# Kernel tuning notes

Hardware: AMD Instinct MI355X
Metric: run time of the kernel (lower is better)

Reference implementation:

```python
import jax, jax.numpy as jnp
import numpy as np

C_DIM = 512
N_TOKEN = 256
N_HEADS = 8
TOKEN_DIM = C_DIM // N_HEADS  # 64


def setup_inputs() -> dict:
    key = jax.random.key(0)
    ks = jax.random.split(key, 8)
    s = 1.0 / np.sqrt(C_DIM)
    W0 = jax.random.normal(ks[0], (4, 8192, C_DIM), dtype=jnp.float32)
    # learnable query tokens (xavier-uniform-ish)
    lim = np.sqrt(6.0 / (N_TOKEN + TOKEN_DIM))
    Q = jax.random.uniform(ks[1], (N_HEADS, N_TOKEN, TOKEN_DIM), minval=-lim, maxval=lim, dtype=jnp.float32)
    kv1_w = jax.random.normal(ks[2], (C_DIM, C_DIM), dtype=jnp.float32) * s
    kv1_b = jnp.zeros((C_DIM,), dtype=jnp.float32)
    qkv2_w = jax.random.normal(ks[3], (TOKEN_DIM, 2 * TOKEN_DIM), dtype=jnp.float32) * (1.0 / np.sqrt(TOKEN_DIM))
    q3_w = jax.random.normal(ks[4], (C_DIM, C_DIM), dtype=jnp.float32) * s
    q3_b = jnp.zeros((C_DIM,), dtype=jnp.float32)
    proj_w = jax.random.normal(ks[5], (C_DIM, C_DIM), dtype=jnp.float32) * s
    proj_b = jnp.zeros((C_DIM,), dtype=jnp.float32)
    return {"W0": W0, "Q": Q, "kv1_w": kv1_w, "kv1_b": kv1_b, "qkv2_w": qkv2_w,
            "q3_w": q3_w, "q3_b": q3_b, "proj_w": proj_w, "proj_b": proj_b}


def reference(W0, Q, kv1_w, kv1_b, qkv2_w, q3_w, q3_b, proj_w, proj_b):
    b, n, c = W0.shape
    h, td = N_HEADS, TOKEN_DIM
    scale = 1.0 / np.sqrt(td)
    # stage 1: compress n nodes into n_token tokens per head
    kv1 = (W0 @ kv1_w + kv1_b).reshape(b, n, h, td).transpose(0, 2, 1, 3)  # b h n c
    pw = jnp.einsum('hmc,bhnc->bhmn', Q, kv1) * scale
    pw = jax.nn.softmax(pw, axis=-1)
    proj_token = jnp.einsum('bhmn,bhnc->bhmc', pw, kv1)  # b h m c
    # stage 2: re-project tokens back to nodes
    kv2 = proj_token @ qkv2_w  # b h m 2c
    k, v = kv2[..., :td], kv2[..., td:]
    q3 = (W0 @ q3_w + q3_b).reshape(b, n, h, td).transpose(0, 2, 1, 3)  # b h n c
    rw = jax.nn.softmax(jnp.einsum('bhnc,bhmc->bhnm', q3, k) * scale, axis=-1)
    W = jnp.einsum('bhnm,bhmc->bhnc', rw, v)
    W = W.transpose(0, 2, 1, 3).reshape(b, n, c)  # b n (h c)
    return W @ proj_w + proj_b
```

## Files before the change

### kernel.cpp

```cpp
#include <hip/hip_runtime.h>
#include <hip/hip_bf16.h>


#define NB 4
#define NSEQ 8192
#define CD 512
#define NH 8
#define TD 64
#define NTOK 256
#define NSPLIT 16
#define NKEYS (NSEQ / NSPLIT)

typedef unsigned short u16;
typedef unsigned int u32;
typedef __bf16 bf16x8 __attribute__((ext_vector_type(8)));
typedef float f32x4 __attribute__((ext_vector_type(4)));
typedef float f32x16 __attribute__((ext_vector_type(16)));

__device__ __forceinline__ u16 f2bf(float f){
  __hip_bfloat16 h = __float2bfloat16(f);
  u16 u; __builtin_memcpy(&u, &h, 2); return u;
}
__device__ __forceinline__ bf16x8 ld8(const u16* p){
  bf16x8 r; __builtin_memcpy(&r, p, 16); return r;
}
__device__ __forceinline__ f32x4 mfma16(bf16x8 a, bf16x8 b, f32x4 c){
  return __builtin_amdgcn_mfma_f32_16x16x32_bf16(a, b, c, 0, 0, 0);
}
__device__ __forceinline__ f32x16 mfma32(bf16x8 a, bf16x8 b, f32x16 c){
  return __builtin_amdgcn_mfma_f32_32x32x16_bf16(a, b, c, 0, 0, 0);
}

__global__ void k_cvt(const float* __restrict__ W0, u16* __restrict__ W0b){
  size_t i = (size_t)blockIdx.x * 256 + threadIdx.x;
  float4 v = ((const float4*)W0)[i];
  u16 w[4] = { f2bf(v.x), f2bf(v.y), f2bf(v.z), f2bf(v.w) };
  __builtin_memcpy(W0b + i*4, w, 8);
}

__global__ void k_prep(const float* __restrict__ kv1_w, const float* __restrict__ q3_w,
                       const float* __restrict__ proj_w, const float* __restrict__ Q,
                       u16* __restrict__ kv1_wt, u16* __restrict__ q3_wt,
                       u16* __restrict__ proj_wt, u16* __restrict__ Qb){
  int i = blockIdx.x * 256 + threadIdx.x;
  int k = i >> 9, n = i & 511;
  kv1_wt [n*CD + k] = f2bf(kv1_w[i]);
  q3_wt  [n*CD + k] = f2bf(q3_w[i] * 0.125f);
  proj_wt[n*CD + k] = f2bf(proj_w[i]);
  if (i < NH*NTOK*TD) Qb[i] = f2bf(Q[i] * 0.125f);
}

__global__ __launch_bounds__(256, 2)
void k_gemm_dual(const u16* __restrict__ A, const u16* __restrict__ B1t,
                 const u16* __restrict__ B2t, const float* __restrict__ bias1,
                 const float* __restrict__ bias2, float bscale2,
                 u16* __restrict__ out1, u16* __restrict__ out2){
  __shared__ __attribute__((aligned(16))) u16 As[128][72];
  __shared__ __attribute__((aligned(16))) u16 B1s[128][72];
  __shared__ __attribute__((aligned(16))) u16 B2s[128][72];
  const int tid = threadIdx.x;
  const int lane = tid & 63, wave = tid >> 6;
  const int l15 = lane & 15, lg = lane >> 4;
  const int wm = (wave >> 1) * 64, wn = (wave & 1) * 64;
  const int bm = blockIdx.x, bn = blockIdx.y;
  f32x4 acc1[4][4] = {}, acc2[4][4] = {};

#pragma unroll 1
  for (int k0 = 0; k0 < CD; k0 += 64){
    __syncthreads();
    {
      int r0 = tid >> 3, c8 = (tid & 7) << 3;
#pragma unroll
      for (int rr = 0; rr < 128; rr += 32){
        const u16* srcA = A   + (size_t)(bm*128 + r0 + rr) * CD + k0 + c8;
        int4 va = *(const int4*)srcA;
        __builtin_memcpy(&As[r0 + rr][c8], &va, 16);
        const u16* s1 = B1t + (size_t)(bn*128 + r0 + rr) * CD + k0 + c8;
        int4 v1 = *(const int4*)s1;
        __builtin_memcpy(&B1s[r0 + rr][c8], &v1, 16);
        const u16* s2 = B2t + (size_t)(bn*128 + r0 + rr) * CD + k0 + c8;
        int4 v2 = *(const int4*)s2;
        __builtin_memcpy(&B2s[r0 + rr][c8], &v2, 16);
      }
    }
    __syncthreads();
#pragma unroll
    for (int ks = 0; ks < 2; ks++){
      bf16x8 af[4], b1f[4], b2f[4];
#pragma unroll
      for (int mf = 0; mf < 4; mf++) af[mf]  = ld8(&As[wm + mf*16 + l15][ks*32 + lg*8]);
#pragma unroll
      for (int nf = 0; nf < 4; nf++){
        b1f[nf] = ld8(&B1s[wn + nf*16 + l15][ks*32 + lg*8]);
        b2f[nf] = ld8(&B2s[wn + nf*16 + l15][ks*32 + lg*8]);
      }
#pragma unroll
      for (int mf = 0; mf < 4; mf++)
#pragma unroll
        for (int nf = 0; nf < 4; nf++){
          acc1[mf][nf] = mfma16(af[mf], b1f[nf], acc1[mf][nf]);
          acc2[mf][nf] = mfma16(af[mf], b2f[nf], acc2[mf][nf]);
        }
    }
  }
#pragma unroll
  for (int nf = 0; nf < 4; nf++){
    int col = bn*128 + wn + nf*16 + l15;
    float bv1 = bias1[col];
    float bv2 = bias2[col] * bscale2;
#pragma unroll
    for (int mf = 0; mf < 4; mf++){
      int row = bm*128 + wm + mf*16 + lg*4;
#pragma unroll
      for (int q = 0; q < 4; q++){
        out1[(size_t)(row + q)*CD + col] = f2bf(acc1[mf][nf][q] + bv1);
        out2[(size_t)(row + q)*CD + col] = f2bf(acc2[mf][nf][q] + bv2);
      }
    }
  }
}

template<int OUT_F32>
__global__ __launch_bounds__(256, 2)
void k_gemm512(const u16* __restrict__ A, const u16* __restrict__ Bt,
               const float* __restrict__ bias, float bscale, void* __restrict__ outp){
  __shared__ __attribute__((aligned(16))) u16 As[128][72];
  __shared__ __attribute__((aligned(16))) u16 Bs[128][72];
  const int tid = threadIdx.x;
  const int lane = tid & 63, wave = tid >> 6;
  const int l15 = lane & 15, lg = lane >> 4;
  const int wm = (wave >> 1) * 64, wn = (wave & 1) * 64;
  const int bm = blockIdx.x, bn = blockIdx.y;
  f32x4 acc[4][4] = {};

#pragma unroll 1
  for (int k0 = 0; k0 < CD; k0 += 64){
    __syncthreads();
    {
      int r0 = tid >> 3, c8 = (tid & 7) << 3;
#pragma unroll
      for (int rr = 0; rr < 128; rr += 32){
        const u16* srcA = A  + (size_t)(bm*128 + r0 + rr) * CD + k0 + c8;
        int4 va = *(const int4*)srcA;
        __builtin_memcpy(&As[r0 + rr][c8], &va, 16);
        const u16* srcB = Bt + (size_t)(bn*128 + r0 + rr) * CD + k0 + c8;
        int4 vb = *(const int4*)srcB;
        __builtin_memcpy(&Bs[r0 + rr][c8], &vb, 16);
      }
    }
    __syncthreads();
#pragma unroll
    for (int ks = 0; ks < 2; ks++){
      bf16x8 af[4], bfr[4];
#pragma unroll
      for (int mf = 0; mf < 4; mf++) af[mf]  = ld8(&As[wm + mf*16 + l15][ks*32 + lg*8]);
#pragma unroll
      for (int nf = 0; nf < 4; nf++) bfr[nf] = ld8(&Bs[wn + nf*16 + l15][ks*32 + lg*8]);
#pragma unroll
      for (int mf = 0; mf < 4; mf++)
#pragma unroll
        for (int nf = 0; nf < 4; nf++)
          acc[mf][nf] = mfma16(af[mf], bfr[nf], acc[mf][nf]);
    }
  }
#pragma unroll
  for (int nf = 0; nf < 4; nf++){
    int col = bn*128 + wn + nf*16 + l15;
    float bv = bias[col] * bscale;
#pragma unroll
    for (int mf = 0; mf < 4; mf++){
      int row = bm*128 + wm + mf*16 + lg*4;
#pragma unroll
      for (int q = 0; q < 4; q++){
        float v = acc[mf][nf][q] + bv;
        if constexpr (OUT_F32) ((float*)outp)[(size_t)(row + q)*CD + col] = v;
        else                   ((u16*)outp)[(size_t)(row + q)*CD + col] = f2bf(v);
      }
    }
  }
}

__global__ __launch_bounds__(256, 4)
void k_attn1(const u16* __restrict__ kv1, const u16* __restrict__ Qb,
             float* __restrict__ o_part, float* __restrict__ ml_part){
  __shared__ __attribute__((aligned(16))) u16 kvs[64][72];
  __shared__ __attribute__((aligned(16))) u16 kvts[64][72];
  __shared__ __attribute__((aligned(16))) u16 pws[4][32][72];
  const int tid = threadIdx.x, lane = tid & 63, wave = tid >> 6;
  const int bh = blockIdx.x, mt = blockIdx.y, s = blockIdx.z;
  const int b = bh >> 3, h = bh & 7;
  const int l15 = lane & 15, lg = lane >> 4;
  const int m0 = mt*128 + wave*32;

  bf16x8 qf[2][2];
#pragma unroll
  for (int mf = 0; mf < 2; mf++)
#pragma unroll
    for (int ks = 0; ks < 2; ks++)
      qf[mf][ks] = ld8(Qb + (size_t)(h*NTOK + m0 + mf*16 + l15)*TD + ks*32 + lg*8);

  float mst[2][4], lst[2][4];
  f32x4 oac[2][4] = {};
#pragma unroll
  for (int mf = 0; mf < 2; mf++)
#pragma unroll
    for (int q = 0; q < 4; q++){ mst[mf][q] = -1e30f; lst[mf][q] = 0.f; }

#pragma unroll 1
  for (int c = 0; c < NKEYS/64; c++){
    const int nc = s*NKEYS + c*64;
    __syncthreads();
    {
      int r = tid >> 2, seg = (tid & 3) * 16;
      const u16* src = kv1 + (size_t)(b*NSEQ + nc + r)*CD + h*TD + seg;
      int4 v0 = *(const int4*)src;
      int4 v1 = *(const int4*)(src + 8);
      __builtin_memcpy(&kvs[r][seg],     &v0, 16);
      __builtin_memcpy(&kvs[r][seg + 8], &v1, 16);
      u16 tmp[16];
      __builtin_memcpy(tmp,     &v0, 16);
      __builtin_memcpy(tmp + 8, &v1, 16);
#pragma unroll
      for (int j = 0; j < 16; j++) kvts[seg + j][r] = tmp[j];
    }
    __syncthreads();
    f32x4 d[2][4] = {};
#pragma unroll
    for (int nf = 0; nf < 4; nf++)
#pragma unroll
      for (int ks = 0; ks < 2; ks++){
        bf16x8 kf = ld8(&kvs[nf*16 + l15][ks*32 + lg*8]);
#pragma unroll
        for (int mf = 0; mf < 2; mf++) d[mf][nf] = mfma16(qf[mf][ks], kf, d[mf][nf]);
      }
#pragma unroll
    for (int mf = 0; mf < 2; mf++)
#pragma unroll
      for (int q = 0; q < 4; q++){
        float cm = fmaxf(fmaxf(d[mf][0][q], d[mf][1][q]), fmaxf(d[mf][2][q], d[mf][3][q]));
#pragma unroll
        for (int off = 1; off < 16; off <<= 1) cm = fmaxf(cm, __shfl_xor(cm, off, 64));
        float mnew = fmaxf(mst[mf][q], cm);
        float corr = __expf(mst[mf][q] - mnew);
        float rs = 0.f;
#pragma unroll
        for (int nf = 0; nf < 4; nf++){
          float e = __expf(d[mf][nf][q] - mnew);
          d[mf][nf][q] = e; rs += e;
        }
#pragma unroll
        for (int off = 1; off < 16; off <<= 1) rs += __shfl_xor(rs, off, 64);
        lst[mf][q] = lst[mf][q]*corr + rs;
        mst[mf][q] = mnew;
#pragma unroll
        for (int tf = 0; tf < 4; tf++) oac[mf][tf][q] *= corr;
        int ml = mf*16 + lg*4 + q;
#pragma unroll
        for (int nf = 0; nf < 4; nf++) pws[wave][ml][nf*16 + l15] = f2bf(d[mf][nf][q]);
      }
#pragma unroll
    for (int ks = 0; ks < 2; ks++){
      bf16x8 a[2];
#pragma unroll
      for (int mf = 0; mf < 2; mf++) a[mf] = ld8(&pws[wave][mf*16 + l15][ks*32 + lg*8]);
#pragma unroll
      for (int tf = 0; tf < 4; tf++){
        bf16x8 vf = ld8(&kvts[tf*16 + l15][ks*32 + lg*8]);
#pragma unroll
        for (int mf = 0; mf < 2; mf++) oac[mf][tf] = mfma16(a[mf], vf, oac[mf][tf]);
      }
    }
  }
  const size_t pbase = (size_t)(bh*NSPLIT + s);
#pragma unroll
  for (int mf = 0; mf < 2; mf++)
#pragma unroll
    for (int q = 0; q < 4; q++){
      int m = m0 + mf*16 + lg*4 + q;
#pragma unroll
      for (int tf = 0; tf < 4; tf++)
        o_part[(pbase*NTOK + m)*TD + tf*16 + l15] = oac[mf][tf][q];
      if (l15 == 0){
        ml_part[(pbase*2)*NTOK + m]     = mst[mf][q];
        ml_part[(pbase*2 + 1)*NTOK + m] = lst[mf][q];
      }
    }
}

__global__ __launch_bounds__(256, 2)
void k_comb(const float* __restrict__ o_part, const float* __restrict__ ml_part,
            const float* __restrict__ qkv2_w, u16* __restrict__ kb, u16* __restrict__ vtb){
  __shared__ float w2[TD*2*TD];
  __shared__ float osh[16][68];
  const int tid = threadIdx.x;
  const int bh = blockIdx.x >> 4, mtile = blockIdx.x & 15;
  const int m0 = mtile * 16;
  for (int i = tid; i < TD*2*TD/4; i += 256) ((float4*)w2)[i] = ((const float4*)qkv2_w)[i];

  const int mi = tid >> 4, tj = tid & 15;
  const int m = m0 + mi;
  float M = -1e30f;
#pragma unroll
  for (int s = 0; s < NSPLIT; s++)
    M = fmaxf(M, ml_part[(size_t)((bh*NSPLIT + s)*2)*NTOK + m]);
  float4 acc = make_float4(0.f,0.f,0.f,0.f);
  float denom = 0.f;
#pragma unroll 1
  for (int s = 0; s < NSPLIT; s++){
    size_t base = (size_t)(bh*NSPLIT + s);
    float w = __expf(ml_part[(base*2)*NTOK + m] - M);
    denom += ml_part[(base*2 + 1)*NTOK + m] * w;
    float4 v = ((const float4*)(o_part + (base*NTOK + m)*TD))[tj];
    acc.x += w*v.x; acc.y += w*v.y; acc.z += w*v.z; acc.w += w*v.w;
  }
  float inv = 1.f / denom;
  osh[mi][tj*4+0] = acc.x*inv; osh[mi][tj*4+1] = acc.y*inv;
  osh[mi][tj*4+2] = acc.z*inv; osh[mi][tj*4+3] = acc.w*inv;
  __syncthreads();
  const int j0 = tj * 8;
  float o8[8] = {};
#pragma unroll
  for (int t = 0; t < TD; t++){
    float ov = osh[mi][t];
#pragma unroll
    for (int jj = 0; jj < 8; jj++) o8[jj] += ov * w2[t*2*TD + j0 + jj];
  }
  if (j0 < TD){
#pragma unroll
    for (int jj = 0; jj < 8; jj++)
      kb[(size_t)(bh*NTOK + m)*TD + j0 + jj] = f2bf(o8[jj]);
  } else {
#pragma unroll
    for (int jj = 0; jj < 8; jj++)
      vtb[(size_t)(bh*TD + (j0 - TD + jj))*NTOK + m] = f2bf(o8[jj]);
  }
}

__global__ __launch_bounds__(256, 2)
void k_attn2(const u16* __restrict__ q3, const u16* __restrict__ kb,
             const u16* __restrict__ vtb, u16* __restrict__ Wout){
  __shared__ __attribute__((aligned(16))) u16 buf[32768];
  u16* kbs = buf;
  u16* vts = buf + 16384;
  const int tid = threadIdx.x, lane = tid & 63, wave = tid >> 6;
  const int bh = blockIdx.x >> 6, nt = blockIdx.x & 63;
  const int b = bh >> 3, h = bh & 7;
  const int l31 = lane & 31, hi = lane >> 5;
  const int n0 = nt * 128 + wave * 32;

  bf16x8 bq[4];
#pragma unroll
  for (int ks = 0; ks < 4; ks++)
    bq[ks] = ld8(q3 + (size_t)(b*NSEQ + n0 + l31)*CD + h*TD + ks*16 + hi*8);

  {
    const u16* ksrc = kb + (size_t)bh*NTOK*TD;
#pragma unroll
    for (int it = 0; it < 8; it++){
      int idx = it*256 + tid;
      int r = idx >> 3, g = idx & 7;
      int4 v; __builtin_memcpy(&v, ksrc + r*64 + g*8, 16);
      __builtin_memcpy(kbs + r*64 + ((g ^ (r & 7)) << 3), &v, 16);
    }
    const u16* vsrc = vtb + (size_t)bh*TD*NTOK;
#pragma unroll
    for (int it = 0; it < 8; it++){
      int idx = it*256 + tid;
      int t = idx >> 5, g = idx & 31;
      int4 v; __builtin_memcpy(&v, vsrc + t*256 + g*8, 16);
      __builtin_memcpy(vts + t*256 + ((g ^ (t & 31)) << 3), &v, 16);
    }
  }
  __syncthreads();

  f32x16 p[8] = {};
  __builtin_amdgcn_s_setprio(1);
#pragma unroll
  for (int kt = 0; kt < 8; kt++){
#pragma unroll
    for (int ks = 0; ks < 4; ks++){
      int r = kt*32 + l31, g = ks*2 + hi;
      bf16x8 ak = ld8(kbs + r*64 + ((g ^ (r & 7)) << 3));
      p[kt] = mfma32(ak, bq[ks], p[kt]);
    }
  }
  __builtin_amdgcn_s_setprio(0);

  float mx0 = -1e30f, mx1 = -1e30f, mx2 = -1e30f, mx3 = -1e30f;
#pragma unroll
  for (int kt = 0; kt < 8; kt++){
#pragma unroll
    for (int r = 0; r < 16; r += 4){
      mx0 = fmaxf(mx0, p[kt][r+0]); mx1 = fmaxf(mx1, p[kt][r+1]);
      mx2 = fmaxf(mx2, p[kt][r+2]); mx3 = fmaxf(mx3, p[kt][r+3]);
    }
  }
  float m = fmaxf(fmaxf(mx0, mx1), fmaxf(mx2, mx3));
  m = fmaxf(m, __shfl_xor(m, 32, 64));
  float s0 = 0.f, s1 = 0.f, s2 = 0.f, s3 = 0.f;
#pragma unroll
  for (int kt = 0; kt < 8; kt++){
#pragma unroll
    for (int r = 0; r < 16; r += 4){
      float e0 = __expf(p[kt][r+0] - m); p[kt][r+0] = e0; s0 += e0;
      float e1 = __expf(p[kt][r+1] - m); p[kt][r+1] = e1; s1 += e1;
      float e2 = __expf(p[kt][r+2] - m); p[kt][r+2] = e2; s2 += e2;
      float e3 = __expf(p[kt][r+3] - m); p[kt][r+3] = e3; s3 += e3;
    }
  }
  float rs = (s0 + s1) + (s2 + s3);
  rs += __shfl_xor(rs, 32, 64);
  const float inv = 1.f / rs;

  f32x16 o0 = {}, o1 = {};
#pragma unroll
  for (int kt = 0; kt < 8; kt++){
    u32 w[8], x[8];
#pragma unroll
    for (int j = 0; j < 8; j++){
      u32 lo = f2bf(p[kt][2*j]);
      u32 hh = f2bf(p[kt][2*j + 1]);
      w[j] = lo | (hh << 16);
    }
#pragma unroll
    for (int j = 0; j < 8; j++) x[j] = __shfl_xor(w[j], 32, 64);
    __builtin_amdgcn_s_setprio(1);
#pragma unroll
    for (int c = 0; c < 2; c++){
      u32 arr[4];
      arr[0] = hi ? x[4*c + 2] : w[4*c + 0];
      arr[1] = hi ? x[4*c + 3] : w[4*c + 1];
      arr[2] = hi ? w[4*c + 2] : x[4*c + 0];
      arr[3] = hi ? w[4*c + 3] : x[4*c + 1];
      bf16x8 pb; __builtin_memcpy(&pb, arr, 16);
      int g = kt*4 + c*2 + hi;
      bf16x8 av0 = ld8(vts + l31*256        + ((g ^ l31) << 3));
      bf16x8 av1 = ld8(vts + (l31+32)*256   + ((g ^ l31) << 3));
      o0 = mfma32(av0, pb, o0);
      o1 = mfma32(av1, pb, o1);
    }
    __builtin_amdgcn_s_setprio(0);
  }

  __syncthreads();
  u16 (*osh)[32][68] = (u16 (*)[32][68])buf;
#pragma unroll
  for (int r = 0; r < 16; r++){
    int row = (r & 3) + 8*(r >> 2) + 4*hi;
    osh[wave][l31][row]      = f2bf(o0[r] * inv);
    osh[wave][l31][32 + row] = f2bf(o1[r] * inv);
  }
  const u16* src = &osh[wave][l31][hi*32];
  int4 v0, v1, v2, v3;
  __builtin_memcpy(&v0, src,      16);
  __builtin_memcpy(&v1, src + 8,  16);
  __builtin_memcpy(&v2, src + 16, 16);
  __builtin_memcpy(&v3, src + 24, 16);
  u16* dst = Wout + (size_t)(b*NSEQ + n0 + l31)*CD + h*TD + hi*32;
  __builtin_memcpy(dst,      &v0, 16);
  __builtin_memcpy(dst + 8,  &v1, 16);
  __builtin_memcpy(dst + 16, &v2, 16);
  __builtin_memcpy(dst + 24, &v3, 16);
}

extern "C" void kernel_launch(void* const* d_in, const int* in_sizes, int n_in,
                              void* d_out, int out_size, void* d_ws, size_t ws_size,
                              hipStream_t stream){
  const float* W0     = (const float*)d_in[0];
  const float* Q      = (const float*)d_in[1];
  const float* kv1_w  = (const float*)d_in[2];
  const float* kv1_b  = (const float*)d_in[3];
  const float* qkv2_w = (const float*)d_in[4];
  const float* q3_w   = (const float*)d_in[5];
  const float* q3_b   = (const float*)d_in[6];
  const float* proj_w = (const float*)d_in[7];
  const float* proj_b = (const float*)d_in[8];
  (void)in_sizes; (void)n_in; (void)out_size; (void)ws_size;

  char* ws = (char*)d_ws;
  u16*   W0b     = (u16*)  (ws);
  u16*   kv1_ws  = (u16*)  (ws + ((size_t)32<<20));
  float* o_part  = (float*)(ws + ((size_t)64<<20));
  float* ml_part = (float*)(ws + ((size_t)96<<20));
  u16*   kv1_wt  = (u16*)  (ws + ((size_t)97<<20));
  u16*   q3_wt   = (u16*)  (ws + ((size_t)97<<20) + (1<<19));
  u16*   proj_wt = (u16*)  (ws + ((size_t)98<<20));
  u16*   Qb      = (u16*)  (ws + ((size_t)98<<20) + (1<<19));
  u16*   kb      = (u16*)  (ws + ((size_t)99<<20));
  u16*   vtb     = (u16*)  (ws + ((size_t)100<<20));
  u16*   W_ws    = (u16*)  (ws + ((size_t)32<<20));
  u16*   q3s     = (u16*)  d_out;

  k_cvt<<<16384, 256, 0, stream>>>(W0, W0b);
  k_prep<<<1024, 256, 0, stream>>>(kv1_w, q3_w, proj_w, Q, kv1_wt, q3_wt, proj_wt, Qb);
  k_gemm_dual<<<dim3(256,4), 256, 0, stream>>>(W0b, kv1_wt, q3_wt, kv1_b, q3_b, 0.125f,
                                               kv1_ws, q3s);
  k_attn1<<<dim3(NB*NH, 2, NSPLIT), 256, 0, stream>>>(kv1_ws, Qb, o_part, ml_part);
  k_comb<<<NB*NH*16, 256, 0, stream>>>(o_part, ml_part, qkv2_w, kb, vtb);
  k_attn2<<<NB*NH*64, 256, 0, stream>>>(q3s, kb, vtb, W_ws);
  k_gemm512<1><<<dim3(256,4), 256, 0, stream>>>(W_ws, proj_wt, proj_b, 1.0f, (void*)d_out);
}
```

Before: 217.1 us.

## Rewrite stage-1 attention with 32x32 MFMA and register-resident softmax probabilities

Restructures the k_attn1 flash-attention loop to use 32x32x16 MFMAs with S transposed (keys as rows), so each lane holds the scores for one query column. Softmax probabilities are converted to bf16 and exchanged between half-waves with a single shuffle, which removes the per-wave LDS staging buffer and the 16-lane shuffle reductions. It also adds a lazy rescale that only updates the running max when it grows by more than 8, and staggers the transposed LDS writes to reduce bank conflicts. Occupancy launch bounds drop from 4 to 3 blocks per CU to allow more registers. The lazy rescale relies on fp32 headroom for exponentials up to e^8.

```diff
diff --git a/kernel.cpp b/kernel.cpp
--- a/kernel.cpp
+++ b/kernel.cpp
@@ -180,38 +180,31 @@
   }
 }
 
-__global__ __launch_bounds__(256, 4)
+__global__ __launch_bounds__(256, 3)
 void k_attn1(const u16* __restrict__ kv1, const u16* __restrict__ Qb,
              float* __restrict__ o_part, float* __restrict__ ml_part){
   __shared__ __attribute__((aligned(16))) u16 kvs[64][72];
   __shared__ __attribute__((aligned(16))) u16 kvts[64][72];
-  __shared__ __attribute__((aligned(16))) u16 pws[4][32][72];
   const int tid = threadIdx.x, lane = tid & 63, wave = tid >> 6;
   const int bh = blockIdx.x, mt = blockIdx.y, s = blockIdx.z;
   const int b = bh >> 3, h = bh & 7;
-  const int l15 = lane & 15, lg = lane >> 4;
+  const int l31 = lane & 31, hi = lane >> 5;
   const int m0 = mt*128 + wave*32;
 
-  bf16x8 qf[2][2];
-#pragma unroll
-  for (int mf = 0; mf < 2; mf++)
-#pragma unroll
-    for (int ks = 0; ks < 2; ks++)
-      qf[mf][ks] = ld8(Qb + (size_t)(h*NTOK + m0 + mf*16 + l15)*TD + ks*32 + lg*8);
-
-  float mst[2][4], lst[2][4];
-  f32x4 oac[2][4] = {};
-#pragma unroll
-  for (int mf = 0; mf < 2; mf++)
-#pragma unroll
-    for (int q = 0; q < 4; q++){ mst[mf][q] = -1e30f; lst[mf][q] = 0.f; }
+  bf16x8 bq[4];
+#pragma unroll
+  for (int ks = 0; ks < 4; ks++)
+    bq[ks] = ld8(Qb + (size_t)(h*NTOK + m0 + l31)*TD + ks*16 + hi*8);
+
+  float mrun = -1e30f, srun = 0.f;
+  f32x16 o0 = {}, o1 = {};
 
 #pragma unroll 1
   for (int c = 0; c < NKEYS/64; c++){
     const int nc = s*NKEYS + c*64;
     __syncthreads();
     {
-      int r = tid >> 2, seg = (tid & 3) * 16;
+      int r = tid >> 2, sg = tid & 3, seg = sg * 16;
       const u16* src = kv1 + (size_t)(b*NSEQ + nc + r)*CD + h*TD + seg;
       int4 v0 = *(const int4*)src;
       int4 v1 = *(const int4*)(src + 8);
@@ -221,70 +214,76 @@
       __builtin_memcpy(tmp,     &v0, 16);
       __builtin_memcpy(tmp + 8, &v1, 16);
 #pragma unroll
-      for (int j = 0; j < 16; j++) kvts[seg + j][r] = tmp[j];
+      for (int j = 0; j < 16; j++){
+        int jj = (j + 2*sg) & 15;
+        kvts[seg + jj][r] = tmp[jj];
+      }
     }
     __syncthreads();
-    f32x4 d[2][4] = {};
-#pragma unroll
-    for (int nf = 0; nf < 4; nf++)
-#pragma unroll
-      for (int ks = 0; ks < 2; ks++){
-        bf16x8 kf = ld8(&kvs[nf*16 + l15][ks*32 + lg*8]);
-#pragma unroll
-        for (int mf = 0; mf < 2; mf++) d[mf][nf] = mfma16(qf[mf][ks], kf, d[mf][nf]);
-      }
-#pragma unroll
-    for (int mf = 0; mf < 2; mf++)
-#pragma unroll
-      for (int q = 0; q < 4; q++){
-        float cm = fmaxf(fmaxf(d[mf][0][q], d[mf][1][q]), fmaxf(d[mf][2][q], d[mf][3][q]));
-#pragma unroll
-        for (int off = 1; off < 16; off <<= 1) cm = fmaxf(cm, __shfl_xor(cm, off, 64));
-        float mnew = fmaxf(mst[mf][q], cm);
-        float corr = __expf(mst[mf][q] - mnew);
-        float rs = 0.f;
-#pragma unroll
-        for (int nf = 0; nf < 4; nf++){
-          float e = __expf(d[mf][nf][q] - mnew);
-          d[mf][nf][q] = e; rs += e;
-        }
-#pragma unroll
-        for (int off = 1; off < 16; off <<= 1) rs += __shfl_xor(rs, off, 64);
-        lst[mf][q] = lst[mf][q]*corr + rs;
-        mst[mf][q] = mnew;
-#pragma unroll
-        for (int tf = 0; tf < 4; tf++) oac[mf][tf][q] *= corr;
-        int ml = mf*16 + lg*4 + q;
-#pragma unroll
-        for (int nf = 0; nf < 4; nf++) pws[wave][ml][nf*16 + l15] = f2bf(d[mf][nf][q]);
-      }
-#pragma unroll
-    for (int ks = 0; ks < 2; ks++){
-      bf16x8 a[2];
-#pragma unroll
-      for (int mf = 0; mf < 2; mf++) a[mf] = ld8(&pws[wave][mf*16 + l15][ks*32 + lg*8]);
-#pragma unroll
-      for (int tf = 0; tf < 4; tf++){
-        bf16x8 vf = ld8(&kvts[tf*16 + l15][ks*32 + lg*8]);
-#pragma unroll
-        for (int mf = 0; mf < 2; mf++) oac[mf][tf] = mfma16(a[mf], vf, oac[mf][tf]);
-      }
-    }
-  }
+#pragma unroll
+    for (int sub = 0; sub < 2; sub++){
+      f32x16 t = {};
+#pragma unroll
+      for (int ks = 0; ks < 4; ks++){
+        bf16x8 ak = ld8(&kvs[sub*32 + l31][ks*16 + hi*8]);
+        t = mfma32(ak, bq[ks], t);
+      }
+      float c0 = fmaxf(fmaxf(t[0], t[1]),  fmaxf(t[2], t[3]));
+      float c1 = fmaxf(fmaxf(t[4], t[5]),  fmaxf(t[6], t[7]));
+      float c2 = fmaxf(fmaxf(t[8], t[9]),  fmaxf(t[10], t[11]));
+      float c3 = fmaxf(fmaxf(t[12], t[13]), fmaxf(t[14], t[15]));
+      float cm = fmaxf(fmaxf(c0, c1), fmaxf(c2, c3));
+      cm = fmaxf(cm, __shfl_xor(cm, 32, 64));
+      if (!__all(cm <= mrun + 8.f)){
+        float mnew = fmaxf(mrun, cm);
+        float corr = __expf(mrun - mnew);
+        srun *= corr;
+#pragma unroll
+        for (int r = 0; r < 16; r++){ o0[r] *= corr; o1[r] *= corr; }
+        mrun = mnew;
+      }
+      u32 w[8], x[8];
+      float ls = 0.f;
+#pragma unroll
+      for (int j = 0; j < 8; j++){
+        float e0 = __expf(t[2*j]     - mrun);
+        float e1 = __expf(t[2*j + 1] - mrun);
+        ls += e0 + e1;
+        w[j] = (u32)f2bf(e0) | ((u32)f2bf(e1) << 16);
+      }
+      srun += ls;
+#pragma unroll
+      for (int j = 0; j < 8; j++) x[j] = __shfl_xor(w[j], 32, 64);
+#pragma unroll
+      for (int c2i = 0; c2i < 2; c2i++){
+        u32 arr[4];
+        arr[0] = hi ? x[4*c2i + 2] : w[4*c2i + 0];
+        arr[1] = hi ? x[4*c2i + 3] : w[4*c2i + 1];
+        arr[2] = hi ? w[4*c2i + 2] : x[4*c2i + 0];
+        arr[3] = hi ? w[4*c2i + 3] : x[4*c2i + 1];
+        bf16x8 pb; __builtin_memcpy(&pb, arr, 16);
+        bf16x8 av0 = ld8(&kvts[l31][sub*32 + c2i*16 + hi*8]);
+        bf16x8 av1 = ld8(&kvts[l31 + 32][sub*32 + c2i*16 + hi*8]);
+        o0 = mfma32(av0, pb, o0);
+        o1 = mfma32(av1, pb, o1);
+      }
+    }
+  }
+  float rs = srun + __shfl_xor(srun, 32, 64);
+
   const size_t pbase = (size_t)(bh*NSPLIT + s);
-#pragma unroll
-  for (int mf = 0; mf < 2; mf++)
-#pragma unroll
-    for (int q = 0; q < 4; q++){
-      int m = m0 + mf*16 + lg*4 + q;
-#pragma unroll
-      for (int tf = 0; tf < 4; tf++)
-        o_part[(pbase*NTOK + m)*TD + tf*16 + l15] = oac[mf][tf][q];
-      if (l15 == 0){
-        ml_part[(pbase*2)*NTOK + m]     = mst[mf][q];
-        ml_part[(pbase*2 + 1)*NTOK + m] = lst[mf][q];
-      }
-    }
+  float* qrow = o_part + (pbase*NTOK + m0 + l31)*TD;
+#pragma unroll
+  for (int g = 0; g < 4; g++){
+    float4 v0 = make_float4(o0[4*g+0], o0[4*g+1], o0[4*g+2], o0[4*g+3]);
+    *(float4*)(qrow + 8*g + 4*hi) = v0;
+    float4 v1 = make_float4(o1[4*g+0], o1[4*g+1], o1[4*g+2], o1[4*g+3]);
+    *(float4*)(qrow + 32 + 8*g + 4*hi) = v1;
+  }
+  if (hi == 0){
+    ml_part[(pbase*2)*NTOK + m0 + l31]     = mrun;
+    ml_part[(pbase*2 + 1)*NTOK + m0 + l31] = rs;
+  }
 }
 
 __global__ __launch_bounds__(256, 2)
```

New measurement: 213.6 us. No clear change (-1.6%).
